# Kernel optimization log

Hardware: AMD Instinct MI355X
Metric: run time of the kernel (lower is better)

Reference implementation:

```python
import jax, jax.numpy as jnp
import numpy as np

HIDDEN, HEADS, HEAD_DIM = 1024, 16, 64
BSZ, SEQ = 2, 2048
SCALE = HEAD_DIM ** (-0.5)
CAUSAL = True


def setup_inputs() -> dict:
    key = jax.random.key(0)
    ks = jax.random.split(key, 7)
    inner = HEADS * HEAD_DIM
    init = lambda k, shape: jax.random.normal(k, shape, dtype=jnp.float32) * (shape[0] ** -0.5)
    return {
        "query": jax.random.normal(ks[0], (BSZ, SEQ, HIDDEN), dtype=jnp.float32),
        "key": jax.random.normal(ks[1], (BSZ, SEQ, HIDDEN), dtype=jnp.float32),
        "value": jax.random.normal(ks[2], (BSZ, SEQ, HIDDEN), dtype=jnp.float32),
        "w_q": init(ks[3], (HIDDEN, inner)),  # stored [in, out]
        "w_k": init(ks[4], (HIDDEN, inner)),
        "w_v": init(ks[5], (HIDDEN, inner)),
        "w_o": init(ks[6], (inner, HIDDEN)),
    }


def reference(query, key, value, w_q, w_k, w_v, w_o):
    bsz, q_len, _ = query.shape
    k_len = key.shape[1]

    def split_heads(x):  # [b, s, h*d] -> [b, h, s, d]
        return x.reshape(x.shape[0], x.shape[1], HEADS, HEAD_DIM).transpose(0, 2, 1, 3)

    q = split_heads(query @ w_q)
    k = split_heads(key @ w_k)
    v = split_heads(value @ w_v)

    scores = jnp.einsum("bhqd,bhkd->bhqk", q, k) * SCALE
    if CAUSAL:
        q_pos = jnp.arange(q_len)
        k_pos = jnp.arange(k_len)
        mask = (k_pos[None, :] <= q_pos[:, None]).astype(scores.dtype)
        scores = scores + (1.0 - mask)[None, None, :, :] * -10000.0
    weights = jax.nn.softmax(scores, axis=-1)
    out = jnp.einsum("bhqk,bhkd->bhqd", weights, v)
    out = out.transpose(0, 2, 1, 3).reshape(bsz, q_len, HEADS * HEAD_DIM)
    return out @ w_o
```

## Files before the change

### kernel.cpp

```cpp
#include <hip/hip_runtime.h>


using u16 = unsigned short;
typedef __bf16 bf16x8 __attribute__((ext_vector_type(8)));
typedef short  s16x8  __attribute__((ext_vector_type(8)));
typedef float  f32x4  __attribute__((ext_vector_type(4)));

#define SEQ   2048
#define QSC   0.18033688f

__device__ __forceinline__ u16 to_bf16(float f) {
  return __builtin_bit_cast(u16, (__bf16)f);
}
__device__ __forceinline__ float from_bf16(u16 v) {
  return __builtin_bit_cast(float, ((unsigned)v) << 16);
}
__device__ __forceinline__ bf16x8 frag_cast(s16x8 v) {
  return __builtin_bit_cast(bf16x8, v);
}
__device__ __forceinline__ f32x4 mfma16(bf16x8 a, bf16x8 b, f32x4 c) {
  return __builtin_amdgcn_mfma_f32_16x16x32_bf16(a, b, c, 0, 0, 0);
}
__device__ __forceinline__ void gload_lds16(const void* g, void* l) {
  __builtin_amdgcn_global_load_lds(
      (const __attribute__((address_space(1))) void*)g,
      (__attribute__((address_space(3))) void*)l, 16, 0, 0);
}

__global__ __launch_bounds__(256) void convert_x(const float* __restrict__ q,
                                                 const float* __restrict__ k,
                                                 const float* __restrict__ v,
                                                 u16* __restrict__ out) {
  const float* src = blockIdx.z == 0 ? q : (blockIdx.z == 1 ? k : v);
  u16* dst = out + (size_t)blockIdx.z * 4194304;
  for (int idx = blockIdx.x * 256 + threadIdx.x; idx < 524288; idx += 512 * 256) {
    const float4* p = (const float4*)(src + (size_t)idx * 8);
    float4 a = p[0], b = p[1];
    s16x8 o;
    o[0] = (short)to_bf16(a.x); o[1] = (short)to_bf16(a.y);
    o[2] = (short)to_bf16(a.z); o[3] = (short)to_bf16(a.w);
    o[4] = (short)to_bf16(b.x); o[5] = (short)to_bf16(b.y);
    o[6] = (short)to_bf16(b.z); o[7] = (short)to_bf16(b.w);
    *(s16x8*)(dst + (size_t)idx * 8) = o;
  }
}

__global__ __launch_bounds__(256) void transpose_w(const float* __restrict__ wq,
                                                   const float* __restrict__ wk,
                                                   const float* __restrict__ wv,
                                                   const float* __restrict__ wo,
                                                   u16* __restrict__ wT) {
  __shared__ float tile[32][33];
  const float* src = blockIdx.z == 0 ? wq : blockIdx.z == 1 ? wk
                     : blockIdx.z == 2 ? wv : wo;
  u16* dst = wT + (size_t)blockIdx.z * 1048576;
  const int x0 = blockIdx.x * 32, y0 = blockIdx.y * 32;
  const int tx = threadIdx.x, ty = threadIdx.y;
#pragma unroll
  for (int i = 0; i < 4; ++i)
    tile[ty + i * 8][tx] = src[(size_t)(y0 + ty + i * 8) * 1024 + x0 + tx];
  __syncthreads();
#pragma unroll
  for (int i = 0; i < 4; ++i)
    dst[(size_t)(x0 + ty + i * 8) * 1024 + y0 + tx] = to_bf16(tile[tx][ty + i * 8]);
}

__global__ __launch_bounds__(256) void gemm_qkv(const u16* __restrict__ X,
                                                const u16* __restrict__ WT,
                                                u16* __restrict__ Qb,
                                                u16* __restrict__ Kb,
                                                u16* __restrict__ VTb) {
  __shared__ u16 As[128 * 32];
  __shared__ u16 Bs[128 * 32];
  const int z = blockIdx.z;
  const u16* A = X + (size_t)z * 4194304;
  const u16* BT = WT + (size_t)z * 1048576;
  const int tid = threadIdx.x;
  const int w = tid >> 6, lane = tid & 63;
  const int g = lane >> 4, c = lane & 15;
  const int wr = w >> 1, wc = w & 1;
  const int row0 = blockIdx.x * 128;
  const int n0 = blockIdx.y * 128;

  f32x4 acc[4][4];
#pragma unroll
  for (int i = 0; i < 4; ++i)
#pragma unroll
    for (int j = 0; j < 4; ++j) acc[i][j] = (f32x4){0.f, 0.f, 0.f, 0.f};

  const int sub = lane >> 2;
  const int kk = (lane & 3) * 8;

  for (int kt = 0; kt < 32; ++kt) {
    const int k0 = kt * 32;
#pragma unroll
    for (int it = 0; it < 2; ++it) {
      const int ch = w * 2 + it;
      const int row = ch * 16 + sub;
      gload_lds16(A + (size_t)(row0 + row) * 1024 + k0 + kk, (char*)As + ch * 1024);
      gload_lds16(BT + (size_t)(n0 + row) * 1024 + k0 + kk, (char*)Bs + ch * 1024);
    }
    __syncthreads();

    bf16x8 af[4], bfr[4];
#pragma unroll
    for (int mi = 0; mi < 4; ++mi)
      af[mi] = frag_cast(*(const s16x8*)((const char*)As + (wr * 64 + mi * 16 + c) * 64 + g * 16));
#pragma unroll
    for (int ni = 0; ni < 4; ++ni)
      bfr[ni] = frag_cast(*(const s16x8*)((const char*)Bs + (wc * 64 + ni * 16 + c) * 64 + g * 16));
#pragma unroll
    for (int mi = 0; mi < 4; ++mi)
#pragma unroll
      for (int ni = 0; ni < 4; ++ni)
        acc[mi][ni] = mfma16(af[mi], bfr[ni], acc[mi][ni]);
    __syncthreads();
  }

  const float sc = (z == 0) ? QSC : 1.0f;
#pragma unroll
  for (int mi = 0; mi < 4; ++mi) {
    const int rowb = row0 + wr * 64 + mi * 16 + g * 4;
#pragma unroll
    for (int ni = 0; ni < 4; ++ni) {
      const int col = n0 + wc * 64 + ni * 16 + c;
#pragma unroll
      for (int r = 0; r < 4; ++r) {
        const int row = rowb + r;
        const float v = acc[mi][ni][r] * sc;
        if (z == 2) {
          const int b = row >> 11, s = row & 2047;
          const int hh = col >> 6, d = col & 63;
          VTb[((size_t)((b * 16 + hh) * 64 + d)) * 2048 + s] = to_bf16(v);
        } else {
          u16* C = z == 0 ? Qb : Kb;
          C[(size_t)row * 1024 + col] = to_bf16(v);
        }
      }
    }
  }
}

__global__ __launch_bounds__(256) void gemm_out(const u16* __restrict__ A,
                                                const u16* __restrict__ BT,
                                                float* __restrict__ C) {
  __shared__ u16 As[64 * 32];
  __shared__ u16 Bs[128 * 32];
  const int tid = threadIdx.x;
  const int w = tid >> 6, lane = tid & 63;
  const int g = lane >> 4, c = lane & 15;
  const int wr = w >> 1, wc = w & 1;
  const int row0 = blockIdx.x * 64;
  const int n0 = blockIdx.y * 128;

  f32x4 acc[2][4];
#pragma unroll
  for (int i = 0; i < 2; ++i)
#pragma unroll
    for (int j = 0; j < 4; ++j) acc[i][j] = (f32x4){0.f, 0.f, 0.f, 0.f};

  const int sub = lane >> 2;
  const int kk = (lane & 3) * 8;

  for (int kt = 0; kt < 32; ++kt) {
    const int k0 = kt * 32;
    {
      const int row = w * 16 + sub;
      gload_lds16(A + (size_t)(row0 + row) * 1024 + k0 + kk, (char*)As + w * 1024);
    }
#pragma unroll
    for (int it = 0; it < 2; ++it) {
      const int ch = w * 2 + it;
      const int row = ch * 16 + sub;
      gload_lds16(BT + (size_t)(n0 + row) * 1024 + k0 + kk, (char*)Bs + ch * 1024);
    }
    __syncthreads();

    bf16x8 af[2], bfr[4];
#pragma unroll
    for (int mi = 0; mi < 2; ++mi)
      af[mi] = frag_cast(*(const s16x8*)((const char*)As + (wr * 32 + mi * 16 + c) * 64 + g * 16));
#pragma unroll
    for (int ni = 0; ni < 4; ++ni)
      bfr[ni] = frag_cast(*(const s16x8*)((const char*)Bs + (wc * 64 + ni * 16 + c) * 64 + g * 16));
#pragma unroll
    for (int mi = 0; mi < 2; ++mi)
#pragma unroll
      for (int ni = 0; ni < 4; ++ni)
        acc[mi][ni] = mfma16(af[mi], bfr[ni], acc[mi][ni]);
    __syncthreads();
  }

#pragma unroll
  for (int mi = 0; mi < 2; ++mi) {
    const int rowb = row0 + wr * 32 + mi * 16 + g * 4;
#pragma unroll
    for (int ni = 0; ni < 4; ++ni) {
      const int col = n0 + wc * 64 + ni * 16 + c;
#pragma unroll
      for (int r = 0; r < 4; ++r)
        C[(size_t)(rowb + r) * 1024 + col] = acc[mi][ni][r];
    }
  }
}

__global__ __launch_bounds__(512, 4) void attn_fwd(const u16* __restrict__ Qb,
                                                   const u16* __restrict__ Kb,
                                                   const u16* __restrict__ VTb,
                                                   u16* __restrict__ PO,
                                                   float* __restrict__ ML) {
  __shared__ u16 Ks[2][128 * 64];
  __shared__ u16 VTs[2][64 * 128];

  const int tid = threadIdx.x;
  const int w = tid >> 6, lane = tid & 63;
  const int g = lane >> 4, c = lane & 15;

  const int flat = blockIdx.x + 40 * blockIdx.y;
  const int logical = (flat & 7) * 160 + (flat >> 3);
  const int slice_id = logical % 40;
  const int bh = logical / 40;
  const int b = bh >> 4, h = bh & 15;

  int sid = slice_id, x = 0;
  for (; x < 16; ++x) {
    const int ns_ = (x + 4) >> 2;
    if (sid < ns_) break;
    sid -= ns_;
  }
  const int ns = (x + 4) >> 2;
  const int np = x + 1;
  const int t0 = (sid * np) / ns, t1 = ((sid + 1) * np) / ns;
  const int sg = slice_id + 40 * bh;
  const int q0w = x * 128 + w * 16;

  bf16x8 qfr[2];
#pragma unroll
  for (int ch = 0; ch < 2; ++ch)
    qfr[ch] = frag_cast(*(const s16x8*)(Qb + (size_t)(b * SEQ + q0w + c) * 1024 + h * 64 + ch * 32 + g * 8));

  s16x8 ones_s;
#pragma unroll
  for (int j = 0; j < 8; ++j) ones_s[j] = (short)0x3F80;
  const bf16x8 onesf = frag_cast(ones_s);

  f32x4 oacc[4];
#pragma unroll
  for (int j = 0; j < 4; ++j) oacc[j] = (f32x4){0.f, 0.f, 0.f, 0.f};
  f32x4 lacc = (f32x4){0.f, 0.f, 0.f, 0.f};
  float m_run = -1e30f;

  const int srow = tid >> 3;
  const int scol = (tid & 7) * 8;
  const int vd = tid >> 4;
  const int vcol = (tid & 15) * 8;

  s16x8 kreg[2], vreg[2];
#define LOADKV(T)                                                                              \
  {                                                                                            \
    const int kv0_ = (T)*128;                                                                  \
    _Pragma("unroll") for (int it = 0; it < 2; ++it) {                                         \
      kreg[it] = *(const s16x8*)(Kb + (size_t)(b * SEQ + kv0_ + srow + it * 64) * 1024 +       \
                                 h * 64 + scol);                                               \
      vreg[it] = *(const s16x8*)(VTb + ((size_t)(bh * 64 + vd + it * 32)) * 2048 + kv0_ +      \
                                 vcol);                                                        \
    }                                                                                          \
  }
#define WRITEKV(BUF)                                                                           \
  {                                                                                            \
    _Pragma("unroll") for (int it = 0; it < 2; ++it) {                                         \
      const int rr_ = srow + it * 64;                                                          \
      const int pr_ = (rr_ & 0x63) | ((rr_ & 4) << 2) | ((rr_ & 0x18) >> 1);                   \
      *(s16x8*)((char*)Ks[BUF] + pr_ * 128 + ((scol * 2) ^ ((pr_ & 7) << 4))) = kreg[it];      \
      const int vr_ = vd + it * 32;                                                            \
      *(s16x8*)((char*)VTs[BUF] + vr_ * 256 + ((vcol * 2) ^ ((vr_ & 7) << 4))) = vreg[it];     \
    }                                                                                          \
  }

  LOADKV(t0);
  WRITEKV(0);
  __syncthreads();

  int cur = 0;
  for (int t = t0; t < t1; ++t) {
    const bool pre = (t + 1 < t1);
    if (pre) LOADKV(t + 1);

    const int kv0 = t * 128;
    if (!(kv0 > q0w + 15)) {
      f32x4 sa[8];
#pragma unroll
      for (int i = 0; i < 8; ++i) sa[i] = (f32x4){0.f, 0.f, 0.f, 0.f};
#pragma unroll
      for (int kvf = 0; kvf < 8; ++kvf) {
        const int kr = kvf * 16 + c;
        const int rb = kr * 128, swz = (kr & 7) << 4;
#pragma unroll
        for (int ch = 0; ch < 2; ++ch) {
          const bf16x8 ak = frag_cast(*(const s16x8*)((char*)Ks[cur] + rb + ((ch * 64 + g * 16) ^ swz)));
          sa[kvf] = mfma16(ak, qfr[ch], sa[kvf]);
        }
      }

      float mt = -1e30f;
      if (kv0 + 127 > q0w) {
        const int q_abs = q0w + c;
#pragma unroll
        for (int kvf = 0; kvf < 8; ++kvf) {
          const int kvb = kv0 + (kvf >> 1) * 32 + (kvf & 1) * 4 + 8 * g;
#pragma unroll
          for (int r = 0; r < 4; ++r) {
            float s = sa[kvf][r];
            if (kvb + r > q_abs) s = -30000.f;
            sa[kvf][r] = s;
            mt = fmaxf(mt, s);
          }
        }
      } else {
#pragma unroll
        for (int kvf = 0; kvf < 8; ++kvf)
#pragma unroll
          for (int r = 0; r < 4; ++r) mt = fmaxf(mt, sa[kvf][r]);
      }
      mt = fmaxf(mt, __shfl_xor(mt, 16));
      mt = fmaxf(mt, __shfl_xor(mt, 32));

      if (__any(mt > m_run + 8.f)) {
        const float m_new = fmaxf(m_run, mt);
        const float alpha = __builtin_amdgcn_exp2f(m_run - m_new);
        m_run = m_new;
#pragma unroll
        for (int r = 0; r < 4; ++r) {
          const float ar = __shfl(alpha, g * 4 + r);
#pragma unroll
          for (int df = 0; df < 4; ++df) oacc[df][r] *= ar;
          lacc[r] *= ar;
        }
      }

      s16x8 pk[4];
#pragma unroll
      for (int kvf = 0; kvf < 8; ++kvf)
#pragma unroll
        for (int r = 0; r < 4; ++r) {
          const float p = __builtin_amdgcn_exp2f(sa[kvf][r] - m_run);
          pk[kvf >> 1][(kvf & 1) * 4 + r] = (short)to_bf16(p);
        }

#pragma unroll
      for (int ch = 0; ch < 4; ++ch) {
        const bf16x8 ap = frag_cast(pk[ch]);
#pragma unroll
        for (int df = 0; df < 4; ++df) {
          const int dr = df * 16 + c;
          const bf16x8 bv = frag_cast(*(const s16x8*)((char*)VTs[cur] + dr * 256 +
                                                      ((ch * 64 + g * 16) ^ ((dr & 7) << 4))));
          oacc[df] = mfma16(ap, bv, oacc[df]);
        }
        lacc = mfma16(ap, onesf, lacc);
      }
    }

    if (pre) WRITEKV(cur ^ 1);
    __syncthreads();
    cur ^= 1;
  }

  const size_t pob = (size_t)sg * 8192;
#pragma unroll
  for (int r = 0; r < 4; ++r) {
    const int row = w * 16 + g * 4 + r;
#pragma unroll
    for (int df = 0; df < 4; ++df)
      PO[pob + row * 64 + df * 16 + c] = to_bf16(oacc[df][r]);
  }
  if (g == 0)
    ML[sg * 256 + (w * 16 + c) * 2 + 0] = m_run;
  if (c == 0) {
#pragma unroll
    for (int r = 0; r < 4; ++r)
      ML[sg * 256 + (w * 16 + g * 4 + r) * 2 + 1] = lacc[r];
  }
}

__global__ __launch_bounds__(512) void attn_merge(const u16* __restrict__ PO,
                                                  const float* __restrict__ ML,
                                                  u16* __restrict__ Ob) {
  const int x = blockIdx.x, bh = blockIdx.y;
  const int b = bh >> 4, h = bh & 15;
  const int tid = threadIdx.x;
  const int row = tid >> 2, c0 = (tid & 3) << 4;

  int base = 0;
  for (int xp = 0; xp < x; ++xp) base += (xp + 4) >> 2;
  const int ns = (x + 4) >> 2;
  const int sg0 = base + 40 * bh;

  float m[4], l[4], a[4];
  float M = -3e38f;
  for (int i = 0; i < ns; ++i) {
    m[i] = ML[(sg0 + i) * 256 + row * 2 + 0];
    l[i] = ML[(sg0 + i) * 256 + row * 2 + 1];
    M = fmaxf(M, m[i]);
  }
  float denom = 0.f;
  for (int i = 0; i < ns; ++i) {
    a[i] = __builtin_amdgcn_exp2f(m[i] - M);
    denom += a[i] * l[i];
  }
  const float inv = 1.f / denom;

  float o[16];
#pragma unroll
  for (int j = 0; j < 16; ++j) o[j] = 0.f;
  for (int i = 0; i < ns; ++i) {
    const float s = a[i] * inv;
    const u16* p = PO + (size_t)(sg0 + i) * 8192 + row * 64 + c0;
    const s16x8 v0 = *(const s16x8*)p;
    const s16x8 v1 = *(const s16x8*)(p + 8);
#pragma unroll
    for (int j = 0; j < 8; ++j) {
      o[j] += s * from_bf16((u16)v0[j]);
      o[8 + j] += s * from_bf16((u16)v1[j]);
    }
  }

  s16x8 lo, hi;
#pragma unroll
  for (int j = 0; j < 8; ++j) {
    lo[j] = (short)to_bf16(o[j]);
    hi[j] = (short)to_bf16(o[8 + j]);
  }
  u16* dst = Ob + (size_t)(b * SEQ + x * 128 + row) * 1024 + h * 64 + c0;
  *(s16x8*)dst = lo;
  *(s16x8*)(dst + 8) = hi;
}

extern "C" void kernel_launch(void* const* d_in, const int* in_sizes, int n_in,
                              void* d_out, int out_size, void* d_ws, size_t ws_size,
                              hipStream_t stream) {
  const float* query = (const float*)d_in[0];
  const float* key_ = (const float*)d_in[1];
  const float* value = (const float*)d_in[2];
  const float* w_q = (const float*)d_in[3];
  const float* w_k = (const float*)d_in[4];
  const float* w_v = (const float*)d_in[5];
  const float* w_o = (const float*)d_in[6];

  char* ws = (char*)d_ws;
  u16* xq = (u16*)(ws + 0);
  u16* PO = (u16*)(ws + 0);
  u16* wT = (u16*)(ws + 25165824);
  float* ML = (float*)(ws + 25165824);
  u16* Qb = (u16*)(ws + 33554432);
  u16* Kb = (u16*)(ws + 41943040);
  u16* VTb = (u16*)(ws + 50331648);
  u16* Ob = (u16*)(ws + 58720256);

  convert_x<<<dim3(512, 1, 3), 256, 0, stream>>>(query, key_, value, xq);
  transpose_w<<<dim3(32, 32, 4), dim3(32, 8), 0, stream>>>(w_q, w_k, w_v, w_o, wT);
  gemm_qkv<<<dim3(32, 8, 3), 256, 0, stream>>>(xq, wT, Qb, Kb, VTb);
  attn_fwd<<<dim3(40, 32), 512, 0, stream>>>(Qb, Kb, VTb, PO, ML);
  attn_merge<<<dim3(16, 32), 512, 0, stream>>>(PO, ML, Ob);
  gemm_out<<<dim3(64, 8), 256, 0, stream>>>(Ob, wT + 3145728, (float*)d_out);
}
```

Measured before the change: 121.7 us.

## Swizzle LDS tiles in GEMMs and swap operands for V projection

Applies an XOR swizzle to the k-chunk placement in shared memory for both the QKV and output GEMMs, so fragment reads from LDS avoid bank conflicts. For the V projection it also swaps the operand roles (weights as A, activations as B), so the transposed V^T store walks consecutive sequence positions along columns and coalesces better. This relies on the grid dimensions for z==2 matching the swapped roles, which holds because both extents are multiples of 128.

```diff
diff --git a/kernel.cpp b/kernel.cpp
--- a/kernel.cpp
+++ b/kernel.cpp
@@ -73,14 +73,24 @@
   __shared__ u16 As[128 * 32];
   __shared__ u16 Bs[128 * 32];
   const int z = blockIdx.z;
-  const u16* A = X + (size_t)z * 4194304;
-  const u16* BT = WT + (size_t)z * 1048576;
+  const u16* A;
+  const u16* BT;
+  int row0, n0;
+  if (z == 2) {
+    A = WT + 2097152;
+    BT = X + 8388608;
+    row0 = blockIdx.y * 128;
+    n0 = blockIdx.x * 128;
+  } else {
+    A = X + (size_t)z * 4194304;
+    BT = WT + (size_t)z * 1048576;
+    row0 = blockIdx.x * 128;
+    n0 = blockIdx.y * 128;
+  }
   const int tid = threadIdx.x;
   const int w = tid >> 6, lane = tid & 63;
   const int g = lane >> 4, c = lane & 15;
   const int wr = w >> 1, wc = w & 1;
-  const int row0 = blockIdx.x * 128;
-  const int n0 = blockIdx.y * 128;
 
   f32x4 acc[4][4];
 #pragma unroll
@@ -89,7 +99,9 @@
     for (int j = 0; j < 4; ++j) acc[i][j] = (f32x4){0.f, 0.f, 0.f, 0.f};
 
   const int sub = lane >> 2;
-  const int kk = (lane & 3) * 8;
+  const int kq = lane & 3;
+  const int ksrc = (kq ^ ((sub >> 1) & 3)) * 8;
+  const int fsw = ((c >> 1) & 3);
 
   for (int kt = 0; kt < 32; ++kt) {
     const int k0 = kt * 32;
@@ -97,18 +109,18 @@
     for (int it = 0; it < 2; ++it) {
       const int ch = w * 2 + it;
       const int row = ch * 16 + sub;
-      gload_lds16(A + (size_t)(row0 + row) * 1024 + k0 + kk, (char*)As + ch * 1024);
-      gload_lds16(BT + (size_t)(n0 + row) * 1024 + k0 + kk, (char*)Bs + ch * 1024);
+      gload_lds16(A + (size_t)(row0 + row) * 1024 + k0 + ksrc, (char*)As + ch * 1024);
+      gload_lds16(BT + (size_t)(n0 + row) * 1024 + k0 + ksrc, (char*)Bs + ch * 1024);
     }
     __syncthreads();
 
     bf16x8 af[4], bfr[4];
 #pragma unroll
     for (int mi = 0; mi < 4; ++mi)
-      af[mi] = frag_cast(*(const s16x8*)((const char*)As + (wr * 64 + mi * 16 + c) * 64 + g * 16));
+      af[mi] = frag_cast(*(const s16x8*)((const char*)As + (wr * 64 + mi * 16 + c) * 64 + ((g ^ fsw) << 4)));
 #pragma unroll
     for (int ni = 0; ni < 4; ++ni)
-      bfr[ni] = frag_cast(*(const s16x8*)((const char*)Bs + (wc * 64 + ni * 16 + c) * 64 + g * 16));
+      bfr[ni] = frag_cast(*(const s16x8*)((const char*)Bs + (wc * 64 + ni * 16 + c) * 64 + ((g ^ fsw) << 4)));
 #pragma unroll
     for (int mi = 0; mi < 4; ++mi)
 #pragma unroll
@@ -129,9 +141,9 @@
         const int row = rowb + r;
         const float v = acc[mi][ni][r] * sc;
         if (z == 2) {
-          const int b = row >> 11, s = row & 2047;
-          const int hh = col >> 6, d = col & 63;
-          VTb[((size_t)((b * 16 + hh) * 64 + d)) * 2048 + s] = to_bf16(v);
+          const int hh = row >> 6, d = row & 63;
+          const int bb = col >> 11, s = col & 2047;
+          VTb[((size_t)((bb * 16 + hh) * 64 + d)) * 2048 + s] = to_bf16(v);
         } else {
           u16* C = z == 0 ? Qb : Kb;
           C[(size_t)row * 1024 + col] = to_bf16(v);
@@ -160,29 +172,31 @@
     for (int j = 0; j < 4; ++j) acc[i][j] = (f32x4){0.f, 0.f, 0.f, 0.f};
 
   const int sub = lane >> 2;
-  const int kk = (lane & 3) * 8;
+  const int kq = lane & 3;
+  const int ksrc = (kq ^ ((sub >> 1) & 3)) * 8;
+  const int fsw = ((c >> 1) & 3);
 
   for (int kt = 0; kt < 32; ++kt) {
     const int k0 = kt * 32;
     {
       const int row = w * 16 + sub;
-      gload_lds16(A + (size_t)(row0 + row) * 1024 + k0 + kk, (char*)As + w * 1024);
+      gload_lds16(A + (size_t)(row0 + row) * 1024 + k0 + ksrc, (char*)As + w * 1024);
     }
 #pragma unroll
     for (int it = 0; it < 2; ++it) {
       const int ch = w * 2 + it;
       const int row = ch * 16 + sub;
-      gload_lds16(BT + (size_t)(n0 + row) * 1024 + k0 + kk, (char*)Bs + ch * 1024);
+      gload_lds16(BT + (size_t)(n0 + row) * 1024 + k0 + ksrc, (char*)Bs + ch * 1024);
     }
     __syncthreads();
 
     bf16x8 af[2], bfr[4];
 #pragma unroll
     for (int mi = 0; mi < 2; ++mi)
-      af[mi] = frag_cast(*(const s16x8*)((const char*)As + (wr * 32 + mi * 16 + c) * 64 + g * 16));
+      af[mi] = frag_cast(*(const s16x8*)((const char*)As + (wr * 32 + mi * 16 + c) * 64 + ((g ^ fsw) << 4)));
 #pragma unroll
     for (int ni = 0; ni < 4; ++ni)
-      bfr[ni] = frag_cast(*(const s16x8*)((const char*)Bs + (wc * 64 + ni * 16 + c) * 64 + g * 16));
+      bfr[ni] = frag_cast(*(const s16x8*)((const char*)Bs + (wc * 64 + ni * 16 + c) * 64 + ((g ^ fsw) << 4)));
 #pragma unroll
     for (int mi = 0; mi < 2; ++mi)
 #pragma unroll
```

Result: faster. 117.3 us (-3.6%).
